# Kernel tuning notes

Hardware: AMD Instinct MI355X
Metric: run time of the kernel (lower is better)

## Reference

```python
import jax, jax.numpy as jnp
import numpy as np

NUM_BUCKETS = 1_000_000
DIM = 64
B = 4096
L = 200


def setup_inputs() -> dict:
    key = jax.random.key(0)
    k_w, k_idx, k_len = jax.random.split(key, 3)
    # Embedding table, init N(0, 0.01) as in nn.init.normal_(std=0.01)
    weight = jax.random.normal(k_w, (NUM_BUCKETS, DIM), dtype=jnp.float32) * 0.01
    # Pre-hashed token indices, padded to L per bag
    idx = jax.random.randint(k_idx, (B, L), 0, NUM_BUCKETS, dtype=jnp.int64)
    # Ragged bag lengths in [0, L); length 0 -> output row of zeros (as in torch code)
    lengths = jax.random.randint(k_len, (B,), 0, L, dtype=jnp.int64)
    return {"weight": weight, "idx": idx, "lengths": lengths}


def reference(weight, idx, lengths):
    # mask[b, l] = l < lengths[b]  -- honors ragged bags without a Python loop
    mask = (jnp.arange(L)[None, :] < lengths[:, None])  # [B, L] bool
    gathered = weight[idx]                               # [B, L, D] gather
    summed = jnp.einsum("bld,bl->bd", gathered, mask.astype(weight.dtype))
    denom = jnp.maximum(lengths, 1).astype(weight.dtype)[:, None]  # avoid /0; empty bags stay 0
    return summed / denom  # mode='mean'
```

## Files before the change

kernel.cpp:

```cpp
#include <hip/hip_runtime.h>


#define NUM_BUCKETS 1000000
#define DIM 64
#define BAGS 4096
#define LMAX 200

__global__ __launch_bounds__(64, 8) void hashbag_kernel(
    const float* __restrict__ weight,
    const int* __restrict__ idx,
    const int* __restrict__ lengths,
    float* __restrict__ out)
{
    __shared__ int s_off[LMAX];
    const int b     = blockIdx.x;
    const int lane  = threadIdx.x;
    const int half  = lane >> 5;
    const int dpair = (lane & 31) << 1;
    const int len   = lengths[b];

    const int* bag = idx + (long)b * LMAX;
    for (int l = lane; l < len; l += 64) {
        s_off[l] = bag[l] << 6;
    }
    __syncthreads();

    const float* wbase = weight + dpair;
    float sx = 0.f, sy = 0.f;

    int l = 0;
    const int pair_end = len & ~1;
    for (; l + 16 <= pair_end; l += 16) {
        const int o0 = s_off[l +  0 + half];
        const int o1 = s_off[l +  2 + half];
        const int o2 = s_off[l +  4 + half];
        const int o3 = s_off[l +  6 + half];
        const int o4 = s_off[l +  8 + half];
        const int o5 = s_off[l + 10 + half];
        const int o6 = s_off[l + 12 + half];
        const int o7 = s_off[l + 14 + half];
        const float2 v0 = *(const float2*)(wbase + o0);
        const float2 v1 = *(const float2*)(wbase + o1);
        const float2 v2 = *(const float2*)(wbase + o2);
        const float2 v3 = *(const float2*)(wbase + o3);
        const float2 v4 = *(const float2*)(wbase + o4);
        const float2 v5 = *(const float2*)(wbase + o5);
        const float2 v6 = *(const float2*)(wbase + o6);
        const float2 v7 = *(const float2*)(wbase + o7);
        sx += ((v0.x + v1.x) + (v2.x + v3.x)) + ((v4.x + v5.x) + (v6.x + v7.x));
        sy += ((v0.y + v1.y) + (v2.y + v3.y)) + ((v4.y + v5.y) + (v6.y + v7.y));
    }
    for (; l < pair_end; l += 2) {
        const float2 v = *(const float2*)(wbase + s_off[l + half]);
        sx += v.x;
        sy += v.y;
    }
    if ((len & 1) && half == 0) {
        const float2 v = *(const float2*)(wbase + s_off[len - 1]);
        sx += v.x;
        sy += v.y;
    }

    sx += __shfl(sx, lane ^ 32);
    sy += __shfl(sy, lane ^ 32);

    const float inv = 1.f / (float)((len > 0) ? len : 1);
    if (half == 0) {
        float2 r; r.x = sx * inv; r.y = sy * inv;
        *(float2*)(out + b * DIM + dpair) = r;
    }
}

extern "C" void kernel_launch(void* const* d_in, const int* in_sizes, int n_in,
                              void* d_out, int out_size, void* d_ws, size_t ws_size,
                              hipStream_t stream) {
    const float* weight  = (const float*)d_in[0];
    const int*   idx     = (const int*)d_in[1];
    const int*   lengths = (const int*)d_in[2];
    float*       out     = (float*)d_out;

    hashbag_kernel<<<BAGS, 64, 0, stream>>>(weight, idx, lengths, out);
}
```

Baseline: 312.8 us.

## Split each bag across two waves with float4 row loads and LDS combine

Each bag now uses 128 threads (two waves). Each wave handles half of the bag's indices, and every 16-lane group loads a whole 256-byte row as float4 chunks, so four rows are fetched per wave instruction instead of two. Partial sums are reduced with xor shuffles, then combined across the two waves through shared memory before the mean is written. The aim is more memory-level parallelism per bag and fewer load instructions, at the cost of an extra barrier and the cross-wave reduction.

```diff
diff --git a/kernel.cpp b/kernel.cpp
--- a/kernel.cpp
+++ b/kernel.cpp
@@ -6,68 +6,75 @@
 #define BAGS 4096
 #define LMAX 200
 
-__global__ __launch_bounds__(64, 8) void hashbag_kernel(
+__global__ __launch_bounds__(128, 8) void hashbag_kernel(
     const float* __restrict__ weight,
     const int* __restrict__ idx,
     const int* __restrict__ lengths,
     float* __restrict__ out)
 {
-    __shared__ int s_off[LMAX];
-    const int b     = blockIdx.x;
-    const int lane  = threadIdx.x;
-    const int half  = lane >> 5;
-    const int dpair = (lane & 31) << 1;
-    const int len   = lengths[b];
+    __shared__ int    s_off[LMAX];
+    __shared__ float4 s_part[16];
+
+    const int b    = blockIdx.x;
+    const int tid  = threadIdx.x;
+    const int wave = tid >> 6;
+    const int lane = tid & 63;
+    const int g    = lane >> 4;
+    const int l16  = lane & 15;
+    const int len  = lengths[b];
 
     const int* bag = idx + (long)b * LMAX;
-    for (int l = lane; l < len; l += 64) {
+    for (int l = tid; l < len; l += 128) {
         s_off[l] = bag[l] << 6;
     }
     __syncthreads();
 
-    const float* wbase = weight + dpair;
-    float sx = 0.f, sy = 0.f;
+    const int hl    = (len + 1) >> 1;
+    const int start = wave * hl;
+    const int end   = (len < start + hl) ? len : (start + hl);
 
-    int l = 0;
-    const int pair_end = len & ~1;
-    for (; l + 16 <= pair_end; l += 16) {
-        const int o0 = s_off[l +  0 + half];
-        const int o1 = s_off[l +  2 + half];
-        const int o2 = s_off[l +  4 + half];
-        const int o3 = s_off[l +  6 + half];
-        const int o4 = s_off[l +  8 + half];
-        const int o5 = s_off[l + 10 + half];
-        const int o6 = s_off[l + 12 + half];
-        const int o7 = s_off[l + 14 + half];
-        const float2 v0 = *(const float2*)(wbase + o0);
-        const float2 v1 = *(const float2*)(wbase + o1);
-        const float2 v2 = *(const float2*)(wbase + o2);
-        const float2 v3 = *(const float2*)(wbase + o3);
-        const float2 v4 = *(const float2*)(wbase + o4);
-        const float2 v5 = *(const float2*)(wbase + o5);
-        const float2 v6 = *(const float2*)(wbase + o6);
-        const float2 v7 = *(const float2*)(wbase + o7);
-        sx += ((v0.x + v1.x) + (v2.x + v3.x)) + ((v4.x + v5.x) + (v6.x + v7.x));
-        sy += ((v0.y + v1.y) + (v2.y + v3.y)) + ((v4.y + v5.y) + (v6.y + v7.y));
+    const float* wbase = weight + (l16 << 2);
+    float ax = 0.f, ay = 0.f, az = 0.f, aw = 0.f;
+
+    int r = start + g;
+    for (; r + 12 < end; r += 16) {
+        const int o0 = s_off[r];
+        const int o1 = s_off[r + 4];
+        const int o2 = s_off[r + 8];
+        const int o3 = s_off[r + 12];
+        const float4 v0 = *(const float4*)(wbase + o0);
+        const float4 v1 = *(const float4*)(wbase + o1);
+        const float4 v2 = *(const float4*)(wbase + o2);
+        const float4 v3 = *(const float4*)(wbase + o3);
+        ax += (v0.x + v1.x) + (v2.x + v3.x);
+        ay += (v0.y + v1.y) + (v2.y + v3.y);
+        az += (v0.z + v1.z) + (v2.z + v3.z);
+        aw += (v0.w + v1.w) + (v2.w + v3.w);
     }
-    for (; l < pair_end; l += 2) {
-        const float2 v = *(const float2*)(wbase + s_off[l + half]);
-        sx += v.x;
-        sy += v.y;
-    }
-    if ((len & 1) && half == 0) {
-        const float2 v = *(const float2*)(wbase + s_off[len - 1]);
-        sx += v.x;
-        sy += v.y;
+    for (; r < end; r += 4) {
+        const float4 v = *(const float4*)(wbase + s_off[r]);
+        ax += v.x; ay += v.y; az += v.z; aw += v.w;
     }
 
-    sx += __shfl(sx, lane ^ 32);
-    sy += __shfl(sy, lane ^ 32);
+    ax += __shfl_xor(ax, 16); ay += __shfl_xor(ay, 16);
+    az += __shfl_xor(az, 16); aw += __shfl_xor(aw, 16);
+    ax += __shfl_xor(ax, 32); ay += __shfl_xor(ay, 32);
+    az += __shfl_xor(az, 32); aw += __shfl_xor(aw, 32);
 
-    const float inv = 1.f / (float)((len > 0) ? len : 1);
-    if (half == 0) {
-        float2 r; r.x = sx * inv; r.y = sy * inv;
-        *(float2*)(out + b * DIM + dpair) = r;
+    if (wave == 1 && lane < 16) {
+        float4 p; p.x = ax; p.y = ay; p.z = az; p.w = aw;
+        s_part[l16] = p;
+    }
+    __syncthreads();
+    if (wave == 0 && lane < 16) {
+        const float4 p = s_part[l16];
+        const float inv = 1.f / (float)((len > 0) ? len : 1);
+        float4 o;
+        o.x = (ax + p.x) * inv;
+        o.y = (ay + p.y) * inv;
+        o.z = (az + p.z) * inv;
+        o.w = (aw + p.w) * inv;
+        *(float4*)(out + b * DIM + (l16 << 2)) = o;
     }
 }
 
@@ -79,5 +86,5 @@
     const int*   lengths = (const int*)d_in[2];
     float*       out     = (float*)d_out;
 
-    hashbag_kernel<<<BAGS, 64, 0, stream>>>(weight, idx, lengths, out);
+    hashbag_kernel<<<BAGS, 128, 0, stream>>>(weight, idx, lengths, out);
 }
```

After: 308.8 us. Within noise of the previous version (-1.3%).
